# Performance work log

Measured on AMD Instinct MI355X. Metric: run time of the kernel, lower is better.

Reference implementation:

```python
import jax, jax.numpy as jnp
import numpy as np

V, B, H, NH = 3, 8192, 2048, 16
HD = H // NH
EPS = 1e-5


def setup_inputs() -> dict:
    key = jax.random.key(0)
    ks = jax.random.split(key, 20)
    s = 0.02
    d = {
        "views": jax.random.normal(ks[0], (V, B, H), jnp.float32),
        # per-view query/key/value projections (torch Linear: y = x @ W.T + b)
        "Wq": jax.random.normal(ks[1], (V, H, H)) * s, "bq": jnp.zeros((V, H)),
        "Wk": jax.random.normal(ks[2], (V, H, H)) * s, "bk": jnp.zeros((V, H)),
        "Wv": jax.random.normal(ks[3], (V, H, H)) * s, "bv": jnp.zeros((V, H)),
        # per-view MultiheadAttention internal in_proj (split into q/k/v) and out_proj
        "Wiq": jax.random.normal(ks[4], (V, H, H)) * s, "biq": jnp.zeros((V, H)),
        "Wik": jax.random.normal(ks[5], (V, H, H)) * s, "bik": jnp.zeros((V, H)),
        "Wiv": jax.random.normal(ks[6], (V, H, H)) * s, "biv": jnp.zeros((V, H)),
        "Wo": jax.random.normal(ks[7], (V, H, H)) * s, "bo": jnp.zeros((V, H)),
        # fusion output linear over concatenated views
        "Wout": jax.random.normal(ks[8], (H, V * H)) * s, "bout": jnp.zeros((H,)),
        # LayerNorm
        "gamma": jnp.ones((H,)), "beta": jnp.zeros((H,)),
    }
    return d


def reference(views, Wq, bq, Wk, bk, Wv, bv, Wiq, biq, Wik, bik, Wiv, biv,
              Wo, bo, Wout, bout, gamma, beta):
    # views: [V, B, H]
    # per-view q/k/v projections applied to each view's own embedding
    q = jnp.einsum('vbh,vgh->vbg', views, Wq) + bq[:, None]      # [V,B,H]
    k_all = jnp.einsum('vbh,vgh->vbg', views, Wk) + bk[:, None]  # [V,B,H]
    v_all = jnp.einsum('vbh,vgh->vbg', views, Wv) + bv[:, None]  # [V,B,H]

    # for query view i, keys/values come from all other views (static gather)
    others = jnp.asarray(np.array([[j for j in range(V) if j != i] for i in range(V)]))
    K = k_all[others]   # [V, V-1, B, H]
    Vv = v_all[others]  # [V, V-1, B, H]

    # MultiheadAttention internal in-projections (per query-view i)
    q2 = jnp.einsum('vbh,vgh->vbg', q, Wiq) + biq[:, None]                # [V,B,H]
    k2 = jnp.einsum('vjbh,vgh->vjbg', K, Wik) + bik[:, None, None]        # [V,V-1,B,H]
    v2 = jnp.einsum('vjbh,vgh->vjbg', Vv, Wiv) + biv[:, None, None]       # [V,V-1,B,H]

    qh = q2.reshape(V, B, NH, HD)           # q_len = 1 (squeezed)
    kh = k2.reshape(V, V - 1, B, NH, HD)
    vh = v2.reshape(V, V - 1, B, NH, HD)

    scores = jnp.einsum('vbnd,vjbnd->vbnj', qh, kh) / jnp.sqrt(jnp.float32(HD))
    attn = jax.nn.softmax(scores, axis=-1)  # over the V-1 key views
    ctx = jnp.einsum('vbnj,vjbnd->vbnd', attn, vh).reshape(V, B, H)
    att_out = jnp.einsum('vbh,vgh->vbg', ctx, Wo) + bo[:, None]           # [V,B,H]

    # concat attended outputs per-sample: [B, V*H]
    fused = att_out.transpose(1, 0, 2).reshape(B, V * H)
    projected = fused @ Wout.T + bout

    # residual with first view + LayerNorm (dropout inactive / eval)
    x = views[0] + projected
    mu = jnp.mean(x, axis=-1, keepdims=True)
    var = jnp.mean(jnp.square(x - mu), axis=-1, keepdims=True)
    out = (x - mu) * jax.lax.rsqrt(var + EPS) * gamma + beta
    return out
```

## Files before the change

kernel.cpp:

```cpp
#include <hip/hip_runtime.h>
#include <hip/hip_bf16.h>

typedef __attribute__((ext_vector_type(8))) __bf16 bf16x8;
typedef __attribute__((ext_vector_type(4))) float f32x4;
typedef __hip_bfloat16 bf16_t;

#define BB 8192L
#define HH 2048L
#define BH (8192L*2048L)
#define WUNIT (2048L*2048L)
#define WT (3L*2048L*2048L)
#define LDS_TOTAL 131072

struct SlabMap { int a[6]; int w[6]; };

__device__ __forceinline__ void gload_lds16(const void* g, void* l) {
    __builtin_amdgcn_global_load_lds((__attribute__((address_space(1))) void*)g,
                                     (__attribute__((address_space(3))) void*)l, 16, 0, 0);
}

template<bool OUT_F32, bool FUSEK>
__global__ __launch_bounds__(512, 1)
void gemm256(const bf16_t* __restrict__ A, int lda, long aslab, SlabMap map, int mshift,
             const bf16_t* __restrict__ Bw, int ldb,
             const float* __restrict__ bias,
             void* __restrict__ Cout, int ldc, long cslab, int K)
{
    extern __shared__ char lds[];
    const int tid  = threadIdx.x;
    const int lane = tid & 63;
    const int w    = tid >> 6;
    const int wm   = w >> 2, wn = w & 3;

    const int nwg = (int)gridDim.x;
    const int wid = (int)blockIdx.x;
    const int swz = (wid & 7) * (nwg >> 3) + (wid >> 3);
    const int bx  = swz & 7;
    const int by  = swz >> 3;

    const int  sl    = by >> mshift;
    const long rowA0 = (long)(by & ((1 << mshift) - 1)) * 256;
    const long rowB0 = (long)bx * 256;
    const bf16_t* Ab = FUSEK ? A : (A + (long)map.a[sl] * aslab);
    const bf16_t* Wb = Bw + (long)map.w[sl] * WUNIT;
    const float*  be = bias ? (bias + (long)map.w[sl] * HH) : nullptr;

    const int srow    = tid >> 3;
    const int schunk8 = ((tid & 7) ^ (srow & 7)) * 8;
    const int wuni    = w * 1024;
    const int NK = K >> 6;

    auto stageA = [&](int s) {
        char* dst = lds + (s & 1) * 65536;
        const int k0 = s << 6;
        const bf16_t* Aeff; int ka;
        if constexpr (FUSEK) { Aeff = A + (long)(k0 >> 11) * aslab; ka = k0 & 2047; }
        else                 { Aeff = Ab; ka = k0; }
        #pragma unroll
        for (int i = 0; i < 4; ++i)
            gload_lds16(Aeff + (rowA0 + i*64 + srow) * (long)lda + (ka + schunk8), dst + i*8192 + wuni);
    };
    auto stageB = [&](int s, int q) {
        char* dst = lds + (s & 1) * 65536 + 32768 + q*16384;
        const int k0 = s << 6;
        #pragma unroll
        for (int j = 0; j < 2; ++j)
            gload_lds16(Wb + (rowB0 + q*128 + j*64 + srow) * (long)ldb + (k0 + schunk8), dst + j*8192 + wuni);
    };

    f32x4 acc[8][4];
    const f32x4 zero = {0.f, 0.f, 0.f, 0.f};
    #pragma unroll
    for (int i = 0; i < 8; ++i)
        #pragma unroll
        for (int j = 0; j < 4; ++j) acc[i][j] = zero;

    stageB(0,0); stageB(0,1);
    stageA(0);
    stageB(1,0); stageB(1,1);
    asm volatile("s_waitcnt vmcnt(4)" ::: "memory");
    asm volatile("s_barrier" ::: "memory");

    const int arow16 = wm*128 + (lane & 15);
    const int brow16 = wn*64  + (lane & 15);
    const int kb     = (lane >> 4) * 16;

    #define LDSA(row, kh) (*(const bf16x8*)(bufA + (row)*128 + (((kh)*64 + kb) ^ (((row) & 7) << 4))))
    #define LDSB(row, kh) (*(const bf16x8*)(bufB + (row)*128 + (((kh)*64 + kb) ^ (((row) & 7) << 4))))

    for (int s = 0; s < NK; ++s) {
        char* bufA = lds + (s & 1) * 65536;
        char* bufB = bufA + 32768;
        bf16x8 a[4][2], b0[2][2], b1[2][2];

        if (s + 1 < NK) stageA(s + 1);
        #pragma unroll
        for (int cf = 0; cf < 2; ++cf) {
            const int r = brow16 + cf*16;
            #pragma unroll
            for (int kh = 0; kh < 2; ++kh) b0[cf][kh] = LDSB(r, kh);
        }
        #pragma unroll
        for (int rf = 0; rf < 4; ++rf) {
            const int r = arow16 + rf*16;
            #pragma unroll
            for (int kh = 0; kh < 2; ++kh) a[rf][kh] = LDSA(r, kh);
        }
        __builtin_amdgcn_s_setprio(1);
        #pragma unroll
        for (int kh = 0; kh < 2; ++kh)
            #pragma unroll
            for (int rf = 0; rf < 4; ++rf)
                #pragma unroll
                for (int cf = 0; cf < 2; ++cf)
                    acc[rf][cf] = __builtin_amdgcn_mfma_f32_16x16x32_bf16(a[rf][kh], b0[cf][kh], acc[rf][cf], 0, 0, 0);
        __builtin_amdgcn_s_setprio(0);
        asm volatile("s_barrier" ::: "memory");

        #pragma unroll
        for (int cf = 0; cf < 2; ++cf) {
            const int r = brow16 + 32 + cf*16;
            #pragma unroll
            for (int kh = 0; kh < 2; ++kh) b1[cf][kh] = LDSB(r, kh);
        }
        __builtin_amdgcn_s_setprio(1);
        #pragma unroll
        for (int kh = 0; kh < 2; ++kh)
            #pragma unroll
            for (int rf = 0; rf < 4; ++rf)
                #pragma unroll
                for (int cf = 0; cf < 2; ++cf)
                    acc[rf][2+cf] = __builtin_amdgcn_mfma_f32_16x16x32_bf16(a[rf][kh], b1[cf][kh], acc[rf][2+cf], 0, 0, 0);
        __builtin_amdgcn_s_setprio(0);
        asm volatile("s_barrier" ::: "memory");

        if (s + 2 < NK) stageB(s + 2, 0);
        #pragma unroll
        for (int rf = 0; rf < 4; ++rf) {
            const int r = arow16 + 64 + rf*16;
            #pragma unroll
            for (int kh = 0; kh < 2; ++kh) a[rf][kh] = LDSA(r, kh);
        }
        __builtin_amdgcn_s_setprio(1);
        #pragma unroll
        for (int kh = 0; kh < 2; ++kh)
            #pragma unroll
            for (int rf = 0; rf < 4; ++rf)
                #pragma unroll
                for (int cf = 0; cf < 2; ++cf)
                    acc[4+rf][cf] = __builtin_amdgcn_mfma_f32_16x16x32_bf16(a[rf][kh], b0[cf][kh], acc[4+rf][cf], 0, 0, 0);
        __builtin_amdgcn_s_setprio(0);
        asm volatile("s_barrier" ::: "memory");

        if (s + 2 < NK) stageB(s + 2, 1);
        __builtin_amdgcn_s_setprio(1);
        #pragma unroll
        for (int kh = 0; kh < 2; ++kh)
            #pragma unroll
            for (int rf = 0; rf < 4; ++rf)
                #pragma unroll
                for (int cf = 0; cf < 2; ++cf)
                    acc[4+rf][2+cf] = __builtin_amdgcn_mfma_f32_16x16x32_bf16(a[rf][kh], b1[cf][kh], acc[4+rf][2+cf], 0, 0, 0);
        __builtin_amdgcn_s_setprio(0);
        if (s + 1 < NK) {
            if (s + 2 < NK) asm volatile("s_waitcnt vmcnt(4)" ::: "memory");
            else            asm volatile("s_waitcnt vmcnt(0)" ::: "memory");
            asm volatile("s_barrier" ::: "memory");
        }
    }
    #undef LDSA
    #undef LDSB

    const long crow0 = rowA0 + wm*128 + ((lane >> 4) * 4);
    const int  ccol0 = (int)rowB0 + wn*64 + (lane & 15);
    const long cbase = (long)sl * cslab;
    #pragma unroll
    for (int rf = 0; rf < 8; ++rf) {
        #pragma unroll
        for (int cf = 0; cf < 4; ++cf) {
            const int col = ccol0 + cf*16;
            const float bv = be ? be[col] : 0.f;
            #pragma unroll
            for (int r = 0; r < 4; ++r) {
                const long row = crow0 + rf*16 + r;
                const float val = acc[rf][cf][r] + bv;
                if constexpr (OUT_F32) ((float*)Cout)[cbase + row*(long)ldc + col] = val;
                else ((bf16_t*)Cout)[cbase + row*(long)ldc + col] = __float2bfloat16(val);
            }
        }
    }
}

__global__ __launch_bounds__(256)
void f2b_kernel(const float* __restrict__ in, bf16_t* __restrict__ out, long n)
{
    long i = ((long)blockIdx.x * 256 + threadIdx.x) * 4;
    const long stride = (long)gridDim.x * 256 * 4;
    for (; i < n; i += stride) {
        const float4 v = *(const float4*)(in + i);
        __hip_bfloat162 lo, hi;
        lo.x = __float2bfloat16(v.x); lo.y = __float2bfloat16(v.y);
        hi.x = __float2bfloat16(v.z); hi.y = __float2bfloat16(v.w);
        *(__hip_bfloat162*)(out + i)     = lo;
        *(__hip_bfloat162*)(out + i + 2) = hi;
    }
}

__global__ __launch_bounds__(256)
void f2bT_kernel(const float* __restrict__ in, bf16_t* __restrict__ out)
{
    __shared__ float sm[64][65];
    const int tile = blockIdx.x;
    const int mat  = tile >> 10;
    const int tr   = (tile >> 5) & 31, tc = tile & 31;
    const int lr = threadIdx.x >> 4;
    const int lc = (threadIdx.x & 15) * 4;
    const float* src = in + (long)mat*WUNIT + ((long)tr*64)*2048 + tc*64;
    #pragma unroll
    for (int it = 0; it < 4; ++it) {
        const int r = lr + it*16;
        const float4 v = *(const float4*)(src + (long)r*2048 + lc);
        sm[r][lc] = v.x; sm[r][lc+1] = v.y; sm[r][lc+2] = v.z; sm[r][lc+3] = v.w;
    }
    __syncthreads();
    bf16_t* dst = out + (long)mat*WUNIT + ((long)tc*64)*2048 + tr*64;
    #pragma unroll
    for (int it = 0; it < 4; ++it) {
        const int r = lr + it*16;
        __hip_bfloat162 p0, p1;
        p0.x = __float2bfloat16(sm[lc+0][r]); p0.y = __float2bfloat16(sm[lc+1][r]);
        p1.x = __float2bfloat16(sm[lc+2][r]); p1.y = __float2bfloat16(sm[lc+3][r]);
        *(__hip_bfloat162*)(dst + (long)r*2048 + lc)     = p0;
        *(__hip_bfloat162*)(dst + (long)r*2048 + lc + 2) = p1;
    }
}

__global__ __launch_bounds__(256)
void biasfold_kernel(const float* __restrict__ W2, int ld,
                     const float* __restrict__ b1, const float* __restrict__ badd,
                     float* __restrict__ out, int K)
{
    const int g2 = blockIdx.x;
    const int t  = threadIdx.x;
    float s = 0.f;
    for (int k = t; k < K; k += 256) s += W2[(long)g2*ld + k] * b1[k];
    #pragma unroll
    for (int off = 32; off > 0; off >>= 1) s += __shfl_xor(s, off);
    __shared__ float rs[4];
    if ((t & 63) == 0) rs[t >> 6] = s;
    __syncthreads();
    if (t == 0) out[g2] = rs[0] + rs[1] + rs[2] + rs[3] + badd[g2];
}

__global__ __launch_bounds__(256)
void attn_kernel(const bf16_t* __restrict__ q2, const bf16_t* __restrict__ k2,
                 const bf16_t* __restrict__ v2, bf16_t* __restrict__ ctx, int bshift)
{
    const long gw = (long)blockIdx.x * 4 + (threadIdx.x >> 6);
    const int lane = threadIdx.x & 63;
    const int  v_  = (int)(gw >> (bshift + 4));
    const long rem = gw & ((1L << (bshift + 4)) - 1);
    const long b   = rem >> 4;
    const int  n   = (int)(rem & 15);
    const long base = ((((long)v_ << bshift) + b)) * HH + (long)n * 128 + lane * 2;

    const __hip_bfloat162 qv = *(const __hip_bfloat162*)(q2 + base);
    const float q0 = __bfloat162float(qv.x), q1 = __bfloat162float(qv.y);
    float s[2], va[2], vb[2];
    #pragma unroll
    for (int j = 0; j < 2; ++j) {
        const long kb = ((((long)(v_*2 + j) << bshift) + b)) * HH + (long)n * 128 + lane * 2;
        const __hip_bfloat162 kv = *(const __hip_bfloat162*)(k2 + kb);
        float p = q0 * __bfloat162float(kv.x) + q1 * __bfloat162float(kv.y);
        #pragma unroll
        for (int off = 32; off > 0; off >>= 1) p += __shfl_xor(p, off);
        s[j] = p;
        const __hip_bfloat162 vv = *(const __hip_bfloat162*)(v2 + kb);
        va[j] = __bfloat162float(vv.x); vb[j] = __bfloat162float(vv.y);
    }
    const float scale = 0.08838834764831845f;
    const float s0 = s[0] * scale, s1 = s[1] * scale;
    const float m  = fmaxf(s0, s1);
    const float e0 = expf(s0 - m), e1 = expf(s1 - m);
    const float inv = 1.0f / (e0 + e1);
    const float a0 = e0 * inv, a1 = e1 * inv;
    __hip_bfloat162 o;
    o.x = __float2bfloat16(a0 * va[0] + a1 * va[1]);
    o.y = __float2bfloat16(a0 * vb[0] + a1 * vb[1]);
    *(__hip_bfloat162*)(ctx + base) = o;
}

__global__ __launch_bounds__(256)
void ln_kernel(const float* __restrict__ proj, const float* __restrict__ v0,
               const float* __restrict__ gamma, const float* __restrict__ beta,
               float* __restrict__ out)
{
    const long b = blockIdx.x;
    const int t = threadIdx.x;
    const float* pr = proj + b * HH;
    const float* vw = v0 + b * HH;
    float x[8]; float s = 0.f, s2 = 0.f;
    #pragma unroll
    for (int k = 0; k < 8; ++k) {
        const int idx = t + k * 256;
        x[k] = vw[idx] + pr[idx];
        s += x[k]; s2 += x[k] * x[k];
    }
    #pragma unroll
    for (int off = 32; off > 0; off >>= 1) { s += __shfl_xor(s, off); s2 += __shfl_xor(s2, off); }
    __shared__ float rs[4], rs2[4];
    if ((t & 63) == 0) { rs[t >> 6] = s; rs2[t >> 6] = s2; }
    __syncthreads();
    s  = rs[0] + rs[1] + rs[2] + rs[3];
    s2 = rs2[0] + rs2[1] + rs2[2] + rs2[3];
    const float mu  = s * (1.0f / 2048.0f);
    const float var = s2 * (1.0f / 2048.0f) - mu * mu;
    const float rstd = rsqrtf(var + 1e-5f);
    #pragma unroll
    for (int k = 0; k < 8; ++k) {
        const int idx = t + k * 256;
        out[b * HH + idx] = (x[k] - mu) * rstd * gamma[idx] + beta[idx];
    }
}

extern "C" void kernel_launch(void* const* d_in, const int* in_sizes, int n_in,
                              void* d_out, int out_size, void* d_ws, size_t ws_size,
                              hipStream_t stream)
{
    const float* views = (const float*)d_in[0];
    const float* Wq   = (const float*)d_in[1];  const float* bq   = (const float*)d_in[2];
    const float* Wk   = (const float*)d_in[3];  const float* bk   = (const float*)d_in[4];
    const float* Wv   = (const float*)d_in[5];  const float* bv   = (const float*)d_in[6];
    const float* Wiq  = (const float*)d_in[7];  const float* biq  = (const float*)d_in[8];
    const float* Wik  = (const float*)d_in[9];  const float* bik  = (const float*)d_in[10];
    const float* Wiv  = (const float*)d_in[11]; const float* biv  = (const float*)d_in[12];
    const float* Wo   = (const float*)d_in[13]; const float* bo   = (const float*)d_in[14];
    const float* Wout = (const float*)d_in[15]; const float* bout = (const float*)d_in[16];
    const float* gamma= (const float*)d_in[17]; const float* beta = (const float*)d_in[18];

    static bool attr_set = false;
    if (!attr_set) {
        hipFuncSetAttribute((const void*)gemm256<false,false>,
                            hipFuncAttributeMaxDynamicSharedMemorySize, LDS_TOTAL);
        hipFuncSetAttribute((const void*)gemm256<true,true>,
                            hipFuncAttributeMaxDynamicSharedMemorySize, LDS_TOTAL);
        attr_set = true;
    }

    char* ws = (char*)d_ws;
    bf16_t* WIQ   = (bf16_t*)ws;
    bf16_t* WIK   = WIQ  + 3*WUNIT;
    bf16_t* WIV   = WIK  + 3*WUNIT;
    bf16_t* WOUTB = WIV  + 3*WUNIT;
    bf16_t* WQT   = WOUTB+ 3*WUNIT;
    bf16_t* WKT   = WQT  + 3*WUNIT;
    bf16_t* WVT   = WKT  + 3*WUNIT;
    bf16_t* WOT   = WVT  + 3*WUNIT;
    bf16_t* WQ2   = WOT  + 3*WUNIT;
    bf16_t* WK2   = WQ2  + 3*WUNIT;
    bf16_t* WV2   = WK2  + 6*WUNIT;
    bf16_t* WFIN  = WV2  + 6*WUNIT;
    float*  BQ2   = (float*)(WFIN + 3*WUNIT);
    float*  BK2   = BQ2 + 3*HH;
    float*  BV2   = BK2 + 6*HH;
    float*  BFIN  = BV2 + 6*HH;
    const long WBYTES_ALL = 42L*WUNIT*2 + 16L*HH*4;

    long avail = (long)ws_size - WBYTES_ALL;
    long Bc = 8192;
    while (Bc > 256 && Bc * 73728L > avail) Bc >>= 1;
    const int mshift = __builtin_ctzl((unsigned long)Bc) - 8;
    const int bshift = __builtin_ctzl((unsigned long)Bc);
    const long S1 = Bc * HH;

    char* act = ws + WBYTES_ALL;
    bf16_t* VBF = (bf16_t*)act;
    bf16_t* Q2B = VBF + 3*S1;
    bf16_t* K2  = Q2B + 3*S1;
    bf16_t* V2  = K2  + 6*S1;
    float*  PROJ= (float*)K2;

    const SlabMap mp3  = {{0,1,2,0,0,0},{0,1,2,0,0,0}};
    const SlabMap mp6k = {{1,2,0,2,0,1},{0,1,2,3,4,5}};
    const SlabMap mpfk = {{0,0,1,1,2,2},{1,2,0,2,0,1}};
    const SlabMap mp1  = {{0,0,0,0,0,0},{0,0,0,0,0,0}};
    const int oth[3][2] = {{1,2},{0,2},{0,1}};

    f2b_kernel<<<4096, 256, 0, stream>>>(Wiq,  WIQ,   WT);
    f2b_kernel<<<4096, 256, 0, stream>>>(Wik,  WIK,   WT);
    f2b_kernel<<<4096, 256, 0, stream>>>(Wiv,  WIV,   WT);
    f2b_kernel<<<4096, 256, 0, stream>>>(Wout, WOUTB, WT);
    f2bT_kernel<<<3072, 256, 0, stream>>>(Wq, WQT);
    f2bT_kernel<<<3072, 256, 0, stream>>>(Wk, WKT);
    f2bT_kernel<<<3072, 256, 0, stream>>>(Wv, WVT);
    f2bT_kernel<<<3072, 256, 0, stream>>>(Wo, WOT);

    gemm256<false,false><<<192, 512, LDS_TOTAL, stream>>>(WIQ, 2048, WUNIT, mp3,  3, WQT, 2048, nullptr, (void*)WQ2, 2048, WUNIT, 2048);
    gemm256<false,false><<<384, 512, LDS_TOTAL, stream>>>(WIK, 2048, WUNIT, mpfk, 3, WKT, 2048, nullptr, (void*)WK2, 2048, WUNIT, 2048);
    gemm256<false,false><<<384, 512, LDS_TOTAL, stream>>>(WIV, 2048, WUNIT, mpfk, 3, WVT, 2048, nullptr, (void*)WV2, 2048, WUNIT, 2048);
    gemm256<false,false><<<192, 512, LDS_TOTAL, stream>>>(WOUTB, 6144, 2048, mp3, 3, WOT, 2048, nullptr, (void*)WFIN, 6144, 2048, 2048);

    for (int v = 0; v < 3; ++v)
        biasfold_kernel<<<2048, 256, 0, stream>>>(Wiq + (long)v*WUNIT, 2048, bq + v*HH, biq + v*HH, BQ2 + v*HH, 2048);
    for (int v = 0; v < 3; ++v)
        for (int j = 0; j < 2; ++j) {
            const int p = v*2 + j, o = oth[v][j];
            biasfold_kernel<<<2048, 256, 0, stream>>>(Wik + (long)v*WUNIT, 2048, bk + o*HH, bik + v*HH, BK2 + p*HH, 2048);
            biasfold_kernel<<<2048, 256, 0, stream>>>(Wiv + (long)v*WUNIT, 2048, bv + o*HH, biv + v*HH, BV2 + p*HH, 2048);
        }
    biasfold_kernel<<<2048, 256, 0, stream>>>(Wout, 6144, bo, bout, BFIN, 6144);

    const int nwg3 = 8 * 3 * (int)(Bc >> 8);
    const int nwg6 = 8 * 6 * (int)(Bc >> 8);
    const int nwg1 = 8 * 1 * (int)(Bc >> 8);
    const int vgrid = (int)((S1 / 1024 > 8192) ? 8192 : S1 / 1024);

    for (long b0 = 0; b0 < BB; b0 += Bc) {
        for (int v = 0; v < 3; ++v)
            f2b_kernel<<<vgrid, 256, 0, stream>>>(views + v*BH + b0*HH, VBF + v*S1, S1);
        gemm256<false,false><<<nwg3, 512, LDS_TOTAL, stream>>>(VBF, 2048, S1, mp3,  mshift, WQ2, 2048, BQ2, (void*)Q2B, 2048, S1, 2048);
        gemm256<false,false><<<nwg6, 512, LDS_TOTAL, stream>>>(VBF, 2048, S1, mp6k, mshift, WK2, 2048, BK2, (void*)K2,  2048, S1, 2048);
        gemm256<false,false><<<nwg6, 512, LDS_TOTAL, stream>>>(VBF, 2048, S1, mp6k, mshift, WV2, 2048, BV2, (void*)V2,  2048, S1, 2048);
        attn_kernel<<<(int)(12*Bc), 256, 0, stream>>>(Q2B, K2, V2, VBF, bshift);
        gemm256<true,true><<<nwg1, 512, LDS_TOTAL, stream>>>(VBF, 2048, S1, mp1, mshift, WFIN, 6144, BFIN, (void*)PROJ, 2048, 0, 6144);
        ln_kernel<<<(int)Bc, 256, 0, stream>>>(PROJ, views + b0*HH, gamma, beta, ((float*)d_out) + b0*HH);
    }
}
```

Measured before the change: 1.980 ms.

## Batch prep launches, alias weight scratch with activations, move GEMM barriers before MFMA

Merges the eight weight conversion/transpose launches into two and the sixteen bias-fold launches into one packed kernel, and converts all three views in one launch when the whole batch fits. Reorders the workspace so the temporary bf16 weight copies share space with the activation buffers, which lets the full batch run in one chunk when the workspace is limited. Inside the GEMM K-loop, barriers now sit after the LDS fragment reads and before each MFMA block, with sched_barrier fences, and the final wait/barrier is moved ahead of the last MFMA group. The barrier placement changes how LDS loads overlap with compute and could either hide latency or add stalls.

Result: faster. 1.699 ms (-14.2%).

```diff
diff --git a/kernel.cpp b/kernel.cpp
--- a/kernel.cpp
+++ b/kernel.cpp
@@ -13,6 +13,9 @@
 #define LDS_TOTAL 131072
 
 struct SlabMap { int a[6]; int w[6]; };
+struct Ptrs4 { const float* in[4]; bf16_t* out[4]; };
+struct FoldJob { const float* W2; const float* b1; const float* badd; float* out; int ld; };
+struct FoldPack { FoldJob j[16]; };
 
 __device__ __forceinline__ void gload_lds16(const void* g, void* l) {
     __builtin_amdgcn_global_load_lds((__attribute__((address_space(1))) void*)g,
@@ -106,6 +109,8 @@
             #pragma unroll
             for (int kh = 0; kh < 2; ++kh) a[rf][kh] = LDSA(r, kh);
         }
+        asm volatile("s_barrier" ::: "memory");
+        __builtin_amdgcn_sched_barrier(0);
         __builtin_amdgcn_s_setprio(1);
         #pragma unroll
         for (int kh = 0; kh < 2; ++kh)
@@ -115,7 +120,6 @@
                 for (int cf = 0; cf < 2; ++cf)
                     acc[rf][cf] = __builtin_amdgcn_mfma_f32_16x16x32_bf16(a[rf][kh], b0[cf][kh], acc[rf][cf], 0, 0, 0);
         __builtin_amdgcn_s_setprio(0);
-        asm volatile("s_barrier" ::: "memory");
 
         #pragma unroll
         for (int cf = 0; cf < 2; ++cf) {
@@ -123,6 +127,8 @@
             #pragma unroll
             for (int kh = 0; kh < 2; ++kh) b1[cf][kh] = LDSB(r, kh);
         }
+        asm volatile("s_barrier" ::: "memory");
+        __builtin_amdgcn_sched_barrier(0);
         __builtin_amdgcn_s_setprio(1);
         #pragma unroll
         for (int kh = 0; kh < 2; ++kh)
@@ -132,7 +138,6 @@
                 for (int cf = 0; cf < 2; ++cf)
                     acc[rf][2+cf] = __builtin_amdgcn_mfma_f32_16x16x32_bf16(a[rf][kh], b1[cf][kh], acc[rf][2+cf], 0, 0, 0);
         __builtin_amdgcn_s_setprio(0);
-        asm volatile("s_barrier" ::: "memory");
 
         if (s + 2 < NK) stageB(s + 2, 0);
         #pragma unroll
@@ -141,6 +146,8 @@
             #pragma unroll
             for (int kh = 0; kh < 2; ++kh) a[rf][kh] = LDSA(r, kh);
         }
+        asm volatile("s_barrier" ::: "memory");
+        __builtin_amdgcn_sched_barrier(0);
         __builtin_amdgcn_s_setprio(1);
         #pragma unroll
         for (int kh = 0; kh < 2; ++kh)
@@ -150,9 +157,14 @@
                 for (int cf = 0; cf < 2; ++cf)
                     acc[4+rf][cf] = __builtin_amdgcn_mfma_f32_16x16x32_bf16(a[rf][kh], b0[cf][kh], acc[4+rf][cf], 0, 0, 0);
         __builtin_amdgcn_s_setprio(0);
-        asm volatile("s_barrier" ::: "memory");
 
         if (s + 2 < NK) stageB(s + 2, 1);
+        if (s + 1 < NK) {
+            if (s + 2 < NK) asm volatile("s_waitcnt vmcnt(4)" ::: "memory");
+            else            asm volatile("s_waitcnt vmcnt(0)" ::: "memory");
+            asm volatile("s_barrier" ::: "memory");
+            __builtin_amdgcn_sched_barrier(0);
+        }
         __builtin_amdgcn_s_setprio(1);
         #pragma unroll
         for (int kh = 0; kh < 2; ++kh)
@@ -162,11 +174,6 @@
                 for (int cf = 0; cf < 2; ++cf)
                     acc[4+rf][2+cf] = __builtin_amdgcn_mfma_f32_16x16x32_bf16(a[rf][kh], b1[cf][kh], acc[4+rf][2+cf], 0, 0, 0);
         __builtin_amdgcn_s_setprio(0);
-        if (s + 1 < NK) {
-            if (s + 2 < NK) asm volatile("s_waitcnt vmcnt(4)" ::: "memory");
-            else            asm volatile("s_waitcnt vmcnt(0)" ::: "memory");
-            asm volatile("s_barrier" ::: "memory");
-        }
     }
     #undef LDSA
     #undef LDSB
@@ -207,15 +214,34 @@
 }
 
 __global__ __launch_bounds__(256)
-void f2bT_kernel(const float* __restrict__ in, bf16_t* __restrict__ out)
+void f2b4_kernel(Ptrs4 p)
+{
+    const long total = 4 * WT;
+    long i = ((long)blockIdx.x * 256 + threadIdx.x) * 4;
+    const long stride = (long)gridDim.x * 256 * 4;
+    for (; i < total; i += stride) {
+        const int  t   = (int)(i / WT);
+        const long off = i - (long)t * WT;
+        const float4 v = *(const float4*)(p.in[t] + off);
+        __hip_bfloat162 lo, hi;
+        lo.x = __float2bfloat16(v.x); lo.y = __float2bfloat16(v.y);
+        hi.x = __float2bfloat16(v.z); hi.y = __float2bfloat16(v.w);
+        *(__hip_bfloat162*)(p.out[t] + off)     = lo;
+        *(__hip_bfloat162*)(p.out[t] + off + 2) = hi;
+    }
+}
+
+__global__ __launch_bounds__(256)
+void f2bT4_kernel(Ptrs4 p)
 {
     __shared__ float sm[64][65];
-    const int tile = blockIdx.x;
-    const int mat  = tile >> 10;
-    const int tr   = (tile >> 5) & 31, tc = tile & 31;
+    const int gmat = blockIdx.x >> 10;
+    const int t    = gmat / 3, m = gmat % 3;
+    const int tile = blockIdx.x & 1023;
+    const int tr   = tile >> 5, tc = tile & 31;
     const int lr = threadIdx.x >> 4;
     const int lc = (threadIdx.x & 15) * 4;
-    const float* src = in + (long)mat*WUNIT + ((long)tr*64)*2048 + tc*64;
+    const float* src = p.in[t] + (long)m*WUNIT + ((long)tr*64)*2048 + tc*64;
     #pragma unroll
     for (int it = 0; it < 4; ++it) {
         const int r = lr + it*16;
@@ -223,7 +249,7 @@
         sm[r][lc] = v.x; sm[r][lc+1] = v.y; sm[r][lc+2] = v.z; sm[r][lc+3] = v.w;
     }
     __syncthreads();
-    bf16_t* dst = out + (long)mat*WUNIT + ((long)tc*64)*2048 + tr*64;
+    bf16_t* dst = p.out[t] + (long)m*WUNIT + ((long)tc*64)*2048 + tr*64;
     #pragma unroll
     for (int it = 0; it < 4; ++it) {
         const int r = lr + it*16;
@@ -236,20 +262,19 @@
 }
 
 __global__ __launch_bounds__(256)
-void biasfold_kernel(const float* __restrict__ W2, int ld,
-                     const float* __restrict__ b1, const float* __restrict__ badd,
-                     float* __restrict__ out, int K)
-{
-    const int g2 = blockIdx.x;
+void biasfold_all(FoldPack p)
+{
+    const FoldJob jb = p.j[blockIdx.x >> 11];
+    const int g2 = blockIdx.x & 2047;
     const int t  = threadIdx.x;
     float s = 0.f;
-    for (int k = t; k < K; k += 256) s += W2[(long)g2*ld + k] * b1[k];
+    for (int k = t; k < jb.ld; k += 256) s += jb.W2[(long)g2*jb.ld + k] * jb.b1[k];
     #pragma unroll
     for (int off = 32; off > 0; off >>= 1) s += __shfl_xor(s, off);
     __shared__ float rs[4];
     if ((t & 63) == 0) rs[t >> 6] = s;
     __syncthreads();
-    if (t == 0) out[g2] = rs[0] + rs[1] + rs[2] + rs[3] + badd[g2];
+    if (t == 0) jb.out[g2] = rs[0] + rs[1] + rs[2] + rs[3] + jb.badd[g2];
 }
 
 __global__ __launch_bounds__(256)
@@ -348,7 +373,18 @@
     }
 
     char* ws = (char*)d_ws;
-    bf16_t* WIQ   = (bf16_t*)ws;
+    bf16_t* WQ2  = (bf16_t*)ws;
+    bf16_t* WK2  = WQ2 + 3*WUNIT;
+    bf16_t* WV2  = WK2 + 6*WUNIT;
+    bf16_t* WFIN = WV2 + 6*WUNIT;
+    float*  BQ2  = (float*)(WFIN + 3*WUNIT);
+    float*  BK2  = BQ2 + 3*HH;
+    float*  BV2  = BK2 + 6*HH;
+    float*  BFIN = BV2 + 6*HH;
+    const long FIXED = 18L*WUNIT*2 + 16L*HH*4;
+
+    char* R = ws + FIXED;
+    bf16_t* WIQ   = (bf16_t*)R;
     bf16_t* WIK   = WIQ  + 3*WUNIT;
     bf16_t* WIV   = WIK  + 3*WUNIT;
     bf16_t* WOUTB = WIV  + 3*WUNIT;
@@ -356,25 +392,19 @@
     bf16_t* WKT   = WQT  + 3*WUNIT;
     bf16_t* WVT   = WKT  + 3*WUNIT;
     bf16_t* WOT   = WVT  + 3*WUNIT;
-    bf16_t* WQ2   = WOT  + 3*WUNIT;
-    bf16_t* WK2   = WQ2  + 3*WUNIT;
-    bf16_t* WV2   = WK2  + 6*WUNIT;
-    bf16_t* WFIN  = WV2  + 6*WUNIT;
-    float*  BQ2   = (float*)(WFIN + 3*WUNIT);
-    float*  BK2   = BQ2 + 3*HH;
-    float*  BV2   = BK2 + 6*HH;
-    float*  BFIN  = BV2 + 6*HH;
-    const long WBYTES_ALL = 42L*WUNIT*2 + 16L*HH*4;
-
-    long avail = (long)ws_size - WBYTES_ALL;
+
+    const long scratch = 24L*WUNIT*2;
     long Bc = 8192;
-    while (Bc > 256 && Bc * 73728L > avail) Bc >>= 1;
+    while (Bc > 256) {
+        long need = Bc * 73728L; if (need < scratch) need = scratch;
+        if (FIXED + need <= (long)ws_size) break;
+        Bc >>= 1;
+    }
     const int mshift = __builtin_ctzl((unsigned long)Bc) - 8;
     const int bshift = __builtin_ctzl((unsigned long)Bc);
     const long S1 = Bc * HH;
 
-    char* act = ws + WBYTES_ALL;
-    bf16_t* VBF = (bf16_t*)act;
+    bf16_t* VBF = (bf16_t*)R;
     bf16_t* Q2B = VBF + 3*S1;
     bf16_t* K2  = Q2B + 3*S1;
     bf16_t* V2  = K2  + 6*S1;
@@ -386,29 +416,30 @@
     const SlabMap mp1  = {{0,0,0,0,0,0},{0,0,0,0,0,0}};
     const int oth[3][2] = {{1,2},{0,2},{0,1}};
 
-    f2b_kernel<<<4096, 256, 0, stream>>>(Wiq,  WIQ,   WT);
-    f2b_kernel<<<4096, 256, 0, stream>>>(Wik,  WIK,   WT);
-    f2b_kernel<<<4096, 256, 0, stream>>>(Wiv,  WIV,   WT);
-    f2b_kernel<<<4096, 256, 0, stream>>>(Wout, WOUTB, WT);
-    f2bT_kernel<<<3072, 256, 0, stream>>>(Wq, WQT);
-    f2bT_kernel<<<3072, 256, 0, stream>>>(Wk, WKT);
-    f2bT_kernel<<<3072, 256, 0, stream>>>(Wv, WVT);
-    f2bT_kernel<<<3072, 256, 0, stream>>>(Wo, WOT);
-
+    {
+        Ptrs4 c1 = {{Wiq, Wik, Wiv, Wout}, {WIQ, WIK, WIV, WOUTB}};
+        f2b4_kernel<<<8192, 256, 0, stream>>>(c1);
+        Ptrs4 c2 = {{Wq, Wk, Wv, Wo}, {WQT, WKT, WVT, WOT}};
+        f2bT4_kernel<<<12288, 256, 0, stream>>>(c2);
+    }
     gemm256<false,false><<<192, 512, LDS_TOTAL, stream>>>(WIQ, 2048, WUNIT, mp3,  3, WQT, 2048, nullptr, (void*)WQ2, 2048, WUNIT, 2048);
     gemm256<false,false><<<384, 512, LDS_TOTAL, stream>>>(WIK, 2048, WUNIT, mpfk, 3, WKT, 2048, nullptr, (void*)WK2, 2048, WUNIT, 2048);
     gemm256<false,false><<<384, 512, LDS_TOTAL, stream>>>(WIV, 2048, WUNIT, mpfk, 3, WVT, 2048, nullptr, (void*)WV2, 2048, WUNIT, 2048);
     gemm256<false,false><<<192, 512, LDS_TOTAL, stream>>>(WOUTB, 6144, 2048, mp3, 3, WOT, 2048, nullptr, (void*)WFIN, 6144, 2048, 2048);
 
-    for (int v = 0; v < 3; ++v)
-        biasfold_kernel<<<2048, 256, 0, stream>>>(Wiq + (long)v*WUNIT, 2048, bq + v*HH, biq + v*HH, BQ2 + v*HH, 2048);
-    for (int v = 0; v < 3; ++v)
-        for (int j = 0; j < 2; ++j) {
-            const int p = v*2 + j, o = oth[v][j];
-            biasfold_kernel<<<2048, 256, 0, stream>>>(Wik + (long)v*WUNIT, 2048, bk + o*HH, bik + v*HH, BK2 + p*HH, 2048);
-            biasfold_kernel<<<2048, 256, 0, stream>>>(Wiv + (long)v*WUNIT, 2048, bv + o*HH, biv + v*HH, BV2 + p*HH, 2048);
-        }
-    biasfold_kernel<<<2048, 256, 0, stream>>>(Wout, 6144, bo, bout, BFIN, 6144);
+    {
+        FoldPack fp;
+        for (int v = 0; v < 3; ++v)
+            fp.j[v] = { Wiq + (long)v*WUNIT, bq + v*HH, biq + v*HH, BQ2 + v*HH, 2048 };
+        for (int v = 0; v < 3; ++v)
+            for (int j = 0; j < 2; ++j) {
+                const int p = v*2 + j, o = oth[v][j];
+                fp.j[3 + p] = { Wik + (long)v*WUNIT, bk + o*HH, bik + v*HH, BK2 + p*HH, 2048 };
+                fp.j[9 + p] = { Wiv + (long)v*WUNIT, bv + o*HH, biv + v*HH, BV2 + p*HH, 2048 };
+            }
+        fp.j[15] = { Wout, bo, bout, BFIN, 6144 };
+        biasfold_all<<<32768, 256, 0, stream>>>(fp);
+    }
 
     const int nwg3 = 8 * 3 * (int)(Bc >> 8);
     const int nwg6 = 8 * 6 * (int)(Bc >> 8);
@@ -416,8 +447,12 @@
     const int vgrid = (int)((S1 / 1024 > 8192) ? 8192 : S1 / 1024);
 
     for (long b0 = 0; b0 < BB; b0 += Bc) {
-        for (int v = 0; v < 3; ++v)
-            f2b_kernel<<<vgrid, 256, 0, stream>>>(views + v*BH + b0*HH, VBF + v*S1, S1);
+        if (Bc == 8192) {
+            f2b_kernel<<<8192, 256, 0, stream>>>(views, VBF, 3*BH);
+        } else {
+            for (int v = 0; v < 3; ++v)
+                f2b_kernel<<<vgrid, 256, 0, stream>>>(views + v*BH + b0*HH, VBF + v*S1, S1);
+        }
         gemm256<false,false><<<nwg3, 512, LDS_TOTAL, stream>>>(VBF, 2048, S1, mp3,  mshift, WQ2, 2048, BQ2, (void*)Q2B, 2048, S1, 2048);
         gemm256<false,false><<<nwg6, 512, LDS_TOTAL, stream>>>(VBF, 2048, S1, mp6k, mshift, WK2, 2048, BK2, (void*)K2,  2048, S1, 2048);
         gemm256<false,false><<<nwg6, 512, LDS_TOTAL, stream>>>(VBF, 2048, S1, mp6k, mshift, WV2, 2048, BV2, (void*)V2,  2048, S1, 2048);
```
